# Performance work log

Measured on AMD Instinct MI355X. Metric: run time of the kernel, lower is better.

## Reference

```python
import jax, jax.numpy as jnp
import numpy as np

B, HP, WP = 4, 32, 32
T = HP * WP
C = 768            # n_embd
NH = 24            # n_head
HS = C // NH       # head_size == HEAD_SIZE == 32
E = HS             # TIME_MIX_EXTRA_DIM = HEAD_SIZE
D = 64             # TIME_DECAY_DIM


def setup_inputs() -> dict:
    key = jax.random.key(0)
    ks = jax.random.split(key, 24)
    small = lambda k, sh: jax.random.uniform(k, sh, jnp.float32, -1e-4, 1e-4)
    inp = {
        "x": jax.random.normal(ks[0], (B, T, C), jnp.float32),
        "time_maa_x": jax.random.uniform(ks[1], (1, 1, C), jnp.float32),
        "time_maa_w": jax.random.uniform(ks[2], (1, 1, C), jnp.float32),
        "time_maa_k": jax.random.uniform(ks[3], (1, 1, C), jnp.float32),
        "time_maa_v": jax.random.uniform(ks[4], (1, 1, C), jnp.float32),
        "time_maa_r": jax.random.uniform(ks[5], (1, 1, C), jnp.float32),
        "time_maa_g": jax.random.uniform(ks[6], (1, 1, C), jnp.float32),
        "time_maa_w1": small(ks[7], (C, 5 * E)),
        "time_maa_w2": small(ks[8], (5, E, C)),
        "time_decay": jnp.linspace(-6.0, -1.0, C, dtype=jnp.float32).reshape(1, 1, C),
        "time_decay_w1": small(ks[9], (C, D)),
        "time_decay_w2": small(ks[10], (D, C)),
        "time_faaaa": jax.random.uniform(ks[11], (NH, HS), jnp.float32, -0.1, 0.6),
        "W_r": jax.random.normal(ks[12], (C, C), jnp.float32) * 0.02,
        "W_k": jax.random.normal(ks[13], (C, C), jnp.float32) * 0.02,
        "W_v": jax.random.normal(ks[14], (C, C), jnp.float32) * 0.02,
        "W_g": jax.random.normal(ks[15], (C, C), jnp.float32) * 0.02,
        "W_o": jax.random.normal(ks[16], (C, C), jnp.float32) * 0.02,
        "ln_w": jnp.ones((C,), jnp.float32),
        "ln_b": jnp.zeros((C,), jnp.float32),
        "Hp": HP,
        "Wp": WP,
    }
    return inp


def q_shift(x, H, W):
    """groups_q_shift with K=1, gamma=1/4: quarter-channel 4-direction spatial shift, zero-padded."""
    Bs, Ts, Cs = x.shape
    g = x.reshape(Bs, H, W, Cs)
    c4 = Cs // 4
    a, b, c, d = g[..., :c4], g[..., c4:2 * c4], g[..., 2 * c4:3 * c4], g[..., 3 * c4:]
    a = jnp.pad(a[:, :, :-1], ((0, 0), (0, 0), (1, 0), (0, 0)))  # shift +W (right)
    b = jnp.pad(b[:, :, 1:], ((0, 0), (0, 0), (0, 1), (0, 0)))   # shift -W (left)
    c = jnp.pad(c[:, :-1], ((0, 0), (1, 0), (0, 0), (0, 0)))     # shift +H (down)
    d = jnp.pad(d[:, 1:], ((0, 0), (0, 1), (0, 0), (0, 0)))      # shift -H (up)
    return jnp.concatenate([a, b, c, d], axis=-1).reshape(Bs, Ts, Cs)


def wkv6(r, k, v, w, u):
    """RWKV6 WKV scan. r,k,v,w: (B,T,C); u: (NH,HS). decay = exp(-exp(w))."""
    Bs, Ts, Cs = r.shape
    rh = r.reshape(Bs, Ts, NH, HS)
    kh = k.reshape(Bs, Ts, NH, HS)
    vh = v.reshape(Bs, Ts, NH, HS)
    dh = jnp.exp(-jnp.exp(w)).reshape(Bs, Ts, NH, HS)

    def step(s, ins):
        rt, kt, vt, dt = ins                                   # each (B,NH,HS)
        kv = kt[..., :, None] * vt[..., None, :]               # (B,NH,HS,HS)
        y = jnp.einsum('bhj,bhji->bhi', rt, s + u[None, :, :, None] * kv)
        s = dt[..., :, None] * s + kv
        return s, y

    xs = (rh.transpose(1, 0, 2, 3), kh.transpose(1, 0, 2, 3),
          vh.transpose(1, 0, 2, 3), dh.transpose(1, 0, 2, 3))
    s0 = jnp.zeros((Bs, NH, HS, HS), r.dtype)
    _, ys = jax.lax.scan(step, s0, xs)                          # (T,B,NH,HS)
    return ys.transpose(1, 0, 2, 3).reshape(Bs, Ts, Cs)


def reference(x, time_maa_x, time_maa_w, time_maa_k, time_maa_v, time_maa_r,
              time_maa_g, time_maa_w1, time_maa_w2, time_decay, time_decay_w1,
              time_decay_w2, time_faaaa, W_r, W_k, W_v, W_g, W_o, ln_w, ln_b,
              Hp, Wp):
    Bs, Ts, Cs = x.shape
    xx = q_shift(x, Hp, Wp) - x                                 # token shift delta
    xxx = x + xx * time_maa_x
    xxx = jnp.tanh(xxx @ time_maa_w1).reshape(Bs, Ts, 5, E)
    mix = jnp.einsum('btke,kec->kbtc', xxx, time_maa_w2)        # (5,B,T,C)
    mw, mk, mv, mr, mg = mix[0], mix[1], mix[2], mix[3], mix[4]

    xw = x + xx * (time_maa_w + mw)
    xk = x + xx * (time_maa_k + mk)
    xv = x + xx * (time_maa_v + mv)
    xr = x + xx * (time_maa_r + mr)
    xg = x + xx * (time_maa_g + mg)

    r = xr @ W_r
    k = xk @ W_k
    v = xv @ W_v
    g = jax.nn.silu(xg @ W_g)

    ww = jnp.tanh(xw @ time_decay_w1) @ time_decay_w2
    w = time_decay + ww                                         # data-dependent log-decay

    y = wkv6(r, k, v, w, time_faaaa)

    # ln_x (LayerNorm over channels)
    mu = y.mean(-1, keepdims=True)
    var = ((y - mu) ** 2).mean(-1, keepdims=True)
    yn = (y - mu) / jnp.sqrt(var + 1e-5) * ln_w + ln_b

    return (yn * g) @ W_o
```

## Files before the change

### kernel.cpp

```cpp
#include <hip/hip_runtime.h>
#include <math.h>

#define BB   4
#define TT   1024
#define CC   768
#define NH_  24
#define HS_  32
#define NBH  (BB * NH_)
#define NCH  16
#define CL   64

static constexpr size_t SZ = (size_t)BB * TT * CC;

typedef __attribute__((ext_vector_type(8))) __bf16 bf16x8;
typedef __attribute__((ext_vector_type(4))) float  f32x4;

__device__ __forceinline__ unsigned short f2bf(float f) {
    unsigned u = __float_as_uint(f);
    unsigned r = (u + 0x7FFFu + ((u >> 16) & 1u)) >> 16;
    return (unsigned short)r;
}
__device__ __forceinline__ float bf2f(unsigned short h) {
    return __uint_as_float(((unsigned)h) << 16);
}

__device__ __forceinline__ void gload16(const unsigned short* g, unsigned short* l)
{
    __builtin_amdgcn_global_load_lds(
        (const __attribute__((address_space(1))) void*)(g),
        (__attribute__((address_space(3))) void*)(l),
        16, 0, 0);
}

__device__ __forceinline__ int xcd_swz(int wg, int nwg)
{
    return (wg & 7) * (nwg >> 3) + (wg >> 3);
}

struct TDesc { const float* src; unsigned short* dst; int R, C; };
struct TArgs { TDesc d[8]; };

__global__ __launch_bounds__(256) void transpose_cast(TArgs a)
{
    __shared__ float tile[32][33];
    TDesc t = a.d[blockIdx.z];
    const int tx0 = blockIdx.x * 32, ty0 = blockIdx.y * 32;
    if (tx0 >= t.C || ty0 >= t.R) return;
    const int tx = threadIdx.x & 31, ty = threadIdx.x >> 5;
    #pragma unroll
    for (int dy = 0; dy < 4; ++dy) {
        int rr = ty0 + ty + dy * 8, cc = tx0 + tx;
        tile[ty + dy * 8][tx] = (rr < t.R && cc < t.C) ? t.src[(size_t)rr * t.C + cc] : 0.f;
    }
    __syncthreads();
    #pragma unroll
    for (int dy = 0; dy < 4; ++dy) {
        int cc = tx0 + ty + dy * 8, rr = ty0 + tx;
        if (cc < t.C && rr < t.R)
            t.dst[(size_t)cc * t.R + rr] = f2bf(tile[tx][ty + dy * 8]);
    }
}

__global__ __launch_bounds__(192) void w2fill(const float* __restrict__ w2,
                                              unsigned short* __restrict__ W2t)
{
    const int n = blockIdx.x;
    const int e = threadIdx.x;
    if (e >= 160) return;
    const int kk = n / 768;
    const int c  = n - kk * 768;
    unsigned short val = 0;
    if ((e >> 5) == kk) val = f2bf(w2[(size_t)e * 768 + c]);
    W2t[(size_t)n * 160 + e] = val;
}

__global__ __launch_bounds__(256) void shift_kernel(
    const float* __restrict__ x, const float* __restrict__ maa_x,
    float* __restrict__ xxO, unsigned short* __restrict__ xxxO)
{
    const int tok = blockIdx.x;
    const int t   = tok & (TT - 1);
    const int hh  = t >> 5;
    const int wp  = t & 31;
    const int tid = threadIdx.x;
    const float* xrow = x + (size_t)tok * CC;
    for (int c = tid; c < CC; c += 256) {
        float xc = xrow[c];
        float sh;
        if (c < 192)      sh = (wp > 0)  ? xrow[c - CC]      : 0.f;
        else if (c < 384) sh = (wp < 31) ? xrow[c + CC]      : 0.f;
        else if (c < 576) sh = (hh > 0)  ? xrow[c - 32 * CC] : 0.f;
        else              sh = (hh < 31) ? xrow[c + 32 * CC] : 0.f;
        float xxv = sh - xc;
        size_t o = (size_t)tok * CC + c;
        xxO[o]  = xxv;
        xxxO[o] = f2bf(fmaf(xxv, maa_x[c], xc));
    }
}

template<int KDIM, class Epi>
__device__ __forceinline__ void gemm_core(const unsigned short* __restrict__ A,
                                          const unsigned short* __restrict__ W,
                                          int N, const Epi& epi)
{
    __shared__ __align__(16) unsigned short As[64][40];
    __shared__ __align__(16) unsigned short Bs[64][40];

    const int tid  = threadIdx.x;
    const int lane = tid & 63;
    const int wv   = tid >> 6;
    const int wm   = (wv >> 1) * 32, wn = (wv & 1) * 32;
    const int m0   = blockIdx.y * 64, n0 = blockIdx.x * 64;
    const int srow = tid >> 2, scb = (tid & 3) * 8;
    const int l15  = lane & 15, kb8 = (lane >> 4) * 8;

    f32x4 acc[2][2];
    #pragma unroll
    for (int a = 0; a < 2; ++a)
        #pragma unroll
        for (int b = 0; b < 2; ++b)
            #pragma unroll
            for (int e = 0; e < 4; ++e) acc[a][b][e] = 0.f;

    const unsigned short* aP = A + (size_t)(m0 + srow) * KDIM + scb;
    const unsigned short* bP = W + (size_t)(n0 + srow) * KDIM + scb;
    const bool bvalid = (n0 + srow) < N;

    for (int k0 = 0; k0 < KDIM; k0 += 32) {
        uint4 av = *(const uint4*)(aP + k0);
        uint4 bw = make_uint4(0u, 0u, 0u, 0u);
        if (bvalid) bw = *(const uint4*)(bP + k0);
        *(uint4*)&As[srow][scb] = av;
        *(uint4*)&Bs[srow][scb] = bw;
        __syncthreads();

        bf16x8 a0 = *(const bf16x8*)&As[wm + l15][kb8];
        bf16x8 a1 = *(const bf16x8*)&As[wm + 16 + l15][kb8];
        bf16x8 b0 = *(const bf16x8*)&Bs[wn + l15][kb8];
        bf16x8 b1 = *(const bf16x8*)&Bs[wn + 16 + l15][kb8];
        acc[0][0] = __builtin_amdgcn_mfma_f32_16x16x32_bf16(a0, b0, acc[0][0], 0, 0, 0);
        acc[0][1] = __builtin_amdgcn_mfma_f32_16x16x32_bf16(a0, b1, acc[0][1], 0, 0, 0);
        acc[1][0] = __builtin_amdgcn_mfma_f32_16x16x32_bf16(a1, b0, acc[1][0], 0, 0, 0);
        acc[1][1] = __builtin_amdgcn_mfma_f32_16x16x32_bf16(a1, b1, acc[1][1], 0, 0, 0);
        __syncthreads();
    }

    const int rb_ = m0 + wm + (lane >> 4) * 4;
    #pragma unroll
    for (int mi = 0; mi < 2; ++mi)
        #pragma unroll
        for (int ni = 0; ni < 2; ++ni) {
            int col = n0 + wn + ni * 16 + l15;
            if (col < N) {
                #pragma unroll
                for (int j = 0; j < 4; ++j)
                    epi(rb_ + mi * 16 + j, col, acc[mi][ni][j]);
            }
        }
}

template<int KDIM, int BK, class Epi>
__device__ __forceinline__ void gemm_core128(const unsigned short* __restrict__ A,
                                             const unsigned short* __restrict__ W,
                                             int N, int m0, int n0, const Epi& epi)
{
    __shared__ __align__(16) unsigned short As[128][BK];
    __shared__ __align__(16) unsigned short Bs[128][BK];

    const int tid  = threadIdx.x;
    const int lane = tid & 63;
    const int wv   = tid >> 6;
    const int wm   = (wv >> 1) * 64, wn = (wv & 1) * 64;
    const int l15  = lane & 15, kb8 = (lane >> 4) * 8, rb4 = (lane >> 4) * 4;
    constexpr int RPC = 2048 / BK;
    const int sr = tid / (BK / 8), sq = (tid % (BK / 8)) * 8;

    f32x4 acc[4][4];
    #pragma unroll
    for (int a = 0; a < 4; ++a)
        #pragma unroll
        for (int b = 0; b < 4; ++b)
            #pragma unroll
            for (int e = 0; e < 4; ++e) acc[a][b][e] = 0.f;

    const unsigned short* aP = A + (size_t)(m0 + sr) * KDIM + sq;
    const unsigned short* bP = W + (size_t)(n0 + sr) * KDIM + sq;

    for (int k0 = 0; k0 < KDIM; k0 += BK) {
        #pragma unroll
        for (int ro = 0; ro < 128; ro += RPC) {
            gload16(aP + (size_t)ro * KDIM + k0, &As[ro + sr][sq]);
            gload16(bP + (size_t)ro * KDIM + k0, &Bs[ro + sr][sq]);
        }
        __syncthreads();

        #pragma unroll
        for (int kk = 0; kk < BK; kk += 32) {
            bf16x8 af[4], bfr[4];
            #pragma unroll
            for (int mi = 0; mi < 4; ++mi)
                af[mi] = *(const bf16x8*)&As[wm + mi * 16 + l15][kk + kb8];
            #pragma unroll
            for (int ni = 0; ni < 4; ++ni)
                bfr[ni] = *(const bf16x8*)&Bs[wn + ni * 16 + l15][kk + kb8];
            #pragma unroll
            for (int mi = 0; mi < 4; ++mi)
                #pragma unroll
                for (int ni = 0; ni < 4; ++ni)
                    acc[mi][ni] = __builtin_amdgcn_mfma_f32_16x16x32_bf16(af[mi], bfr[ni], acc[mi][ni], 0, 0, 0);
        }
        __syncthreads();
    }

    const int rbase = m0 + wm + rb4;
    #pragma unroll
    for (int mi = 0; mi < 4; ++mi)
        #pragma unroll
        for (int ni = 0; ni < 4; ++ni) {
            int col = n0 + wn + ni * 16 + l15;
            if (col < N) {
                #pragma unroll
                for (int j = 0; j < 4; ++j)
                    epi(rbase + mi * 16 + j, col, acc[mi][ni][j]);
            }
        }
}

struct EpiTanh {
    unsigned short* O; int ldo;
    __device__ void operator()(int r, int c, float v) const {
        O[(size_t)r * ldo + c] = f2bf(tanhf(v));
    }
};
struct EpiF32 {
    float* O;
    __device__ void operator()(int r, int c, float v) const {
        O[(size_t)r * 768 + c] = v;
    }
};
struct EpiDec {
    const float* td; float* O;
    __device__ void operator()(int r, int c, float v) const {
        O[(size_t)r * 768 + c] = expf(-expf(td[c] + v));
    }
};
struct EpiMix {
    const float* px; const float* pxx;
    const float* maa[5];
    unsigned short* outs[5];
    __device__ void operator()(int r, int c, float v) const {
        int kk = c / 768;
        int cc = c - kk * 768;
        size_t o = (size_t)r * 768 + cc;
        outs[kk][o] = f2bf(fmaf(pxx[o], maa[kk][cc] + v, px[o]));
    }
};
struct EpiRKVG {
    unsigned short* O; bool silu;
    __device__ void operator()(int r, int c, float v) const {
        if (silu) v = v / (1.f + expf(-v));
        O[(size_t)r * 768 + c] = f2bf(v);
    }
};

template<int KDIM, class Epi>
__global__ __launch_bounds__(256) void gemm_one(const unsigned short* __restrict__ A,
                                                const unsigned short* __restrict__ W,
                                                int N, Epi epi)
{
    gemm_core<KDIM>(A, W, N, epi);
}

template<int KDIM, int BK, int NB, class Epi>
__global__ __launch_bounds__(256) void gemm_one128(const unsigned short* __restrict__ A,
                                                   const unsigned short* __restrict__ W,
                                                   int N, Epi epi)
{
    const int idx = xcd_swz(blockIdx.x, gridDim.x);
    const int m0 = (idx / NB) * 128, n0 = (idx % NB) * 128;
    gemm_core128<KDIM, BK>(A, W, N, m0, n0, epi);
}

struct QuadArgs {
    const unsigned short* A[4];
    const unsigned short* W[4];
    unsigned short* O[4];
};
__global__ __launch_bounds__(256) void gemm_quad768(QuadArgs q)
{
    const int idx = xcd_swz(blockIdx.x, 768);
    const int z = idx / 192;
    const int rz = idx - z * 192;
    const int m0 = (rz / 6) * 128, n0 = (rz % 6) * 128;
    EpiRKVG e{q.O[z], z == 3};
    gemm_core128<768, 64>(q.A[z], q.W[z], 768, m0, n0, e);
}

__global__ __launch_bounds__(256) void wkv_local(
    const unsigned short* __restrict__ r, const unsigned short* __restrict__ k,
    const unsigned short* __restrict__ v, const float* __restrict__ dec,
    const float* __restrict__ u, float* __restrict__ y,
    unsigned short* __restrict__ rsb, float* __restrict__ kvt,
    float* __restrict__ dcv)
{
    __shared__ __align__(16) unsigned short rwL[64][40], kwL[64][40];
    __shared__ __align__(16) unsigned short vT0[32][40], vT1[32][40];
    __shared__ __align__(16) unsigned short ksT0[32][40], ksT1[32][40];
    __shared__ __align__(16) unsigned short PL0[64][40], PL1[64][40];
    __shared__ float AL[65][32];
    __shared__ float segprod[8][32];
    __shared__ float dpart[64][4];
    __shared__ float diagL[64];
    __shared__ float uL[32];

    const int c   = blockIdx.x;
    const int bh  = blockIdx.y;
    const int b = bh / NH_, h = bh % NH_;
    const int tid  = threadIdx.x;
    const int lane = tid & 63;
    const int wv   = tid >> 6;
    const int l15  = lane & 15;
    const int kb8  = (lane >> 4) * 8;
    const int rb4  = (lane >> 4) * 4;
    const int tc   = c * CL;

    const size_t base0 = ((size_t)b * TT) * CC + (size_t)h * HS_;

    if (tid < 32) uL[tid] = u[h * HS_ + tid];

    const int lrow = tid >> 2, lq = (tid & 3) * 8;
    const int cj = tid & 31, cseg = tid >> 5;

    {
        size_t gp = base0 + (size_t)(tc + lrow) * CC + lq;
        uint4 rv = *(const uint4*)(r + gp);
        uint4 kv = *(const uint4*)(k + gp);
        uint4 vv = *(const uint4*)(v + gp);
        *(uint4*)&rwL[lrow][lq] = rv;
        *(uint4*)&kwL[lrow][lq] = kv;
        const unsigned short* vp = (const unsigned short*)&vv;
        if (lrow < 32) {
            #pragma unroll
            for (int e = 0; e < 8; ++e) vT0[lq + e][lrow] = vp[e];
        } else {
            #pragma unroll
            for (int e = 0; e < 8; ++e) vT1[lq + e][lrow - 32] = vp[e];
        }
    }
    float dv[8];
    #pragma unroll
    for (int q = 0; q < 8; ++q)
        dv[q] = dec[base0 + (size_t)(tc + cseg * 8 + q) * CC + cj];
    {
        float lp = dv[0];
        #pragma unroll
        for (int q = 1; q < 8; ++q) lp *= dv[q];
        segprod[cseg][cj] = lp;
    }
    __syncthreads();

    {
        const int ptau = tid >> 2, pp = tid & 3;
        float acc = 0.f;
        #pragma unroll
        for (int e = 0; e < 8; ++e) {
            int j = pp * 8 + e;
            acc += bf2f(rwL[ptau][j]) * uL[j] * bf2f(kwL[ptau][j]);
        }
        dpart[ptau][pp] = acc;
    }
    {
        float pre = 1.f;
        #pragma unroll
        for (int s = 0; s < 7; ++s) if (s < cseg) pre *= segprod[s][cj];
        float run = pre;
        #pragma unroll
        for (int q = 0; q < 8; ++q) {
            AL[cseg * 8 + q][cj] = run;
            run *= dv[q];
        }
        if (cseg == 7) AL[64][cj] = run;
    }
    __syncthreads();

    if (tid < 64)
        diagL[tid] = dpart[tid][0] + dpart[tid][1] + dpart[tid][2] + dpart[tid][3];
    if (tid < 32)
        dcv[((size_t)bh * NCH + c) * 32 + tid] = AL[64][tid];

    #pragma unroll
    for (int q = 0; q < 8; ++q) {
        int tau = cseg * 8 + q;
        float a  = AL[tau][cj];
        float ia = 1.f / AL[tau + 1][cj];
        unsigned short rs = f2bf(bf2f(rwL[tau][cj]) * a);
        unsigned short ks = f2bf(bf2f(kwL[tau][cj]) * ia);
        rwL[tau][cj] = rs;
        kwL[tau][cj] = ks;
        if (tau < 32) ksT0[cj][tau] = ks; else ksT1[cj][tau - 32] = ks;
    }
    __syncthreads();

    {
        const int wm = (wv >> 1) * 32, wn = (wv & 1) * 32;
        bf16x8 a0 = *(const bf16x8*)&rwL[wm + l15][kb8];
        bf16x8 a1 = *(const bf16x8*)&rwL[wm + 16 + l15][kb8];
        bf16x8 b0 = *(const bf16x8*)&kwL[wn + l15][kb8];
        bf16x8 b1 = *(const bf16x8*)&kwL[wn + 16 + l15][kb8];
        f32x4 qf[2][2];
        #pragma unroll
        for (int mi = 0; mi < 2; ++mi)
            #pragma unroll
            for (int ni = 0; ni < 2; ++ni)
                #pragma unroll
                for (int e = 0; e < 4; ++e) qf[mi][ni][e] = 0.f;
        qf[0][0] = __builtin_amdgcn_mfma_f32_16x16x32_bf16(a0, b0, qf[0][0], 0, 0, 0);
        qf[0][1] = __builtin_amdgcn_mfma_f32_16x16x32_bf16(a0, b1, qf[0][1], 0, 0, 0);
        qf[1][0] = __builtin_amdgcn_mfma_f32_16x16x32_bf16(a1, b0, qf[1][0], 0, 0, 0);
        qf[1][1] = __builtin_amdgcn_mfma_f32_16x16x32_bf16(a1, b1, qf[1][1], 0, 0, 0);
        #pragma unroll
        for (int mi = 0; mi < 2; ++mi)
            #pragma unroll
            for (int ni = 0; ni < 2; ++ni) {
                const int col = wn + ni * 16 + l15;
                #pragma unroll
                for (int jj = 0; jj < 4; ++jj) {
                    const int row = wm + mi * 16 + rb4 + jj;
                    float val = (col < row) ? qf[mi][ni][jj]
                              : ((col == row) ? diagL[row] : 0.f);
                    unsigned short bvv = f2bf(val);
                    if (col < 32) PL0[row][col] = bvv;
                    else          PL1[row][col - 32] = bvv;
                }
            }
    }
    __syncthreads();

    *(uint4*)(rsb + base0 + (size_t)(tc + lrow) * CC + lq) = *(const uint4*)&rwL[lrow][lq];

    {
        const int mr = wv * 16;
        bf16x8 pa0 = *(const bf16x8*)&PL0[mr + l15][kb8];
        bf16x8 pa1 = *(const bf16x8*)&PL1[mr + l15][kb8];
        #pragma unroll
        for (int ni = 0; ni < 2; ++ni) {
            bf16x8 bv0 = *(const bf16x8*)&vT0[ni * 16 + l15][kb8];
            bf16x8 bv1 = *(const bf16x8*)&vT1[ni * 16 + l15][kb8];
            f32x4 acc;
            #pragma unroll
            for (int e = 0; e < 4; ++e) acc[e] = 0.f;
            acc = __builtin_amdgcn_mfma_f32_16x16x32_bf16(pa0, bv0, acc, 0, 0, 0);
            acc = __builtin_amdgcn_mfma_f32_16x16x32_bf16(pa1, bv1, acc, 0, 0, 0);
            #pragma unroll
            for (int jj = 0; jj < 4; ++jj)
                y[base0 + (size_t)(tc + mr + rb4 + jj) * CC + ni * 16 + l15] = acc[jj];
        }
    }

    {
        const int mi_ = (wv >> 1) * 16, nj = (wv & 1) * 16;
        bf16x8 av0 = *(const bf16x8*)&vT0[mi_ + l15][kb8];
        bf16x8 av1 = *(const bf16x8*)&vT1[mi_ + l15][kb8];
        bf16x8 bk0 = *(const bf16x8*)&ksT0[nj + l15][kb8];
        bf16x8 bk1 = *(const bf16x8*)&ksT1[nj + l15][kb8];
        f32x4 acc;
        #pragma unroll
        for (int e = 0; e < 4; ++e) acc[e] = 0.f;
        acc = __builtin_amdgcn_mfma_f32_16x16x32_bf16(av0, bk0, acc, 0, 0, 0);
        acc = __builtin_amdgcn_mfma_f32_16x16x32_bf16(av1, bk1, acc, 0, 0, 0);
        const int j = nj + l15;
        const size_t sb = ((size_t)bh * NCH + c) << 10;
        #pragma unroll
        for (int jj = 0; jj < 4; ++jj)
            kvt[sb + (size_t)(mi_ + rb4 + jj) * 32 + j] = acc[jj];
    }
}

__global__ __launch_bounds__(256) void wkv_carry(
    const float* __restrict__ kvt, const float* __restrict__ dcv,
    unsigned short* __restrict__ spv)
{
    const int bh = blockIdx.x;
    const int tid = threadIdx.x;
    const int e0 = tid << 2;
    const int j0 = e0 & 31;
    float s0 = 0.f, s1 = 0.f, s2 = 0.f, s3 = 0.f;
    #pragma unroll
    for (int c = 0; c < NCH; ++c) {
        const size_t sb = (size_t)bh * NCH + c;
        float4 kv = *(const float4*)(kvt + (sb << 10) + e0);
        float4 d4 = *(const float4*)(dcv + sb * 32 + j0);
        s0 = d4.x * (s0 + kv.x);
        s1 = d4.y * (s1 + kv.y);
        s2 = d4.z * (s2 + kv.z);
        s3 = d4.w * (s3 + kv.w);
        if (c < NCH - 1) {
            unsigned lo = (unsigned)f2bf(s0) | ((unsigned)f2bf(s1) << 16);
            unsigned hi = (unsigned)f2bf(s2) | ((unsigned)f2bf(s3) << 16);
            *(uint2*)(spv + ((sb + 1) << 10) + e0) = make_uint2(lo, hi);
        }
    }
}

__global__ __launch_bounds__(256) void wkv_stadd(
    const unsigned short* __restrict__ rsb, const unsigned short* __restrict__ spv,
    float* __restrict__ y)
{
    __shared__ __align__(16) unsigned short rsL[64][40];
    __shared__ __align__(16) unsigned short STb[32][40];

    const int c  = blockIdx.x + 1;
    const int bh = blockIdx.y;
    const int b = bh / NH_, h = bh % NH_;
    const int tid = threadIdx.x, lane = tid & 63, wv = tid >> 6;
    const int l15 = lane & 15, kb8 = (lane >> 4) * 8, rb4 = (lane >> 4) * 4;
    const int tc = c * CL;
    const size_t base0 = ((size_t)b * TT) * CC + (size_t)h * HS_;
    const int lrow = tid >> 2, lq = (tid & 3) * 8;

    *(uint4*)&rsL[lrow][lq] = *(const uint4*)(rsb + base0 + (size_t)(tc + lrow) * CC + lq);
    if (tid < 128) {
        int row = tid >> 2, q = (tid & 3) * 8;
        *(uint4*)&STb[row][q] =
            *(const uint4*)(spv + (((size_t)bh * NCH + c) << 10) + (size_t)row * 32 + q);
    }
    __syncthreads();

    const int mr = wv * 16;
    bf16x8 ra = *(const bf16x8*)&rsL[mr + l15][kb8];
    #pragma unroll
    for (int ni = 0; ni < 2; ++ni) {
        bf16x8 bs = *(const bf16x8*)&STb[ni * 16 + l15][kb8];
        f32x4 acc;
        #pragma unroll
        for (int e = 0; e < 4; ++e) acc[e] = 0.f;
        acc = __builtin_amdgcn_mfma_f32_16x16x32_bf16(ra, bs, acc, 0, 0, 0);
        #pragma unroll
        for (int jj = 0; jj < 4; ++jj) {
            size_t gp = base0 + (size_t)(tc + mr + rb4 + jj) * CC + ni * 16 + l15;
            y[gp] += acc[jj];
        }
    }
}

__global__ __launch_bounds__(256) void ln_gate(
    const float* __restrict__ y, const unsigned short* __restrict__ g,
    const float* __restrict__ lnw, const float* __restrict__ lnb,
    unsigned short* __restrict__ z)
{
    __shared__ float sy[CC];
    __shared__ float rbuf[8];
    __shared__ float stats[2];

    const int row = blockIdx.x, tid = threadIdx.x;
    const float* yr = y + (size_t)row * CC;

    float s1 = 0.f, s2 = 0.f;
    #pragma unroll
    for (int q = 0; q < 3; ++q) {
        int c = tid + q * 256;
        float vv = yr[c];
        sy[c] = vv;
        s1 += vv;
        s2 += vv * vv;
    }
    #pragma unroll
    for (int off = 32; off > 0; off >>= 1) {
        s1 += __shfl_down(s1, off);
        s2 += __shfl_down(s2, off);
    }
    const int wid = tid >> 6;
    if ((tid & 63) == 0) { rbuf[wid] = s1; rbuf[4 + wid] = s2; }
    __syncthreads();
    if (tid == 0) {
        float S1 = rbuf[0] + rbuf[1] + rbuf[2] + rbuf[3];
        float S2 = rbuf[4] + rbuf[5] + rbuf[6] + rbuf[7];
        float mu = S1 / (float)CC;
        float var = S2 / (float)CC - mu * mu;
        stats[0] = mu;
        stats[1] = rsqrtf(var + 1e-5f);
    }
    __syncthreads();
    const float mu = stats[0], rstd = stats[1];
    const unsigned short* gr = g + (size_t)row * CC;
    unsigned short* zr = z + (size_t)row * CC;
    #pragma unroll
    for (int q = 0; q < 3; ++q) {
        int c = tid + q * 256;
        zr[c] = f2bf(fmaf((sy[c] - mu) * rstd, lnw[c], lnb[c]) * bf2f(gr[c]));
    }
}

extern "C" void kernel_launch(void* const* d_in, const int* in_sizes, int n_in,
                              void* d_out, int out_size, void* d_ws, size_t ws_size,
                              hipStream_t stream)
{
    const float* x      = (const float*)d_in[0];
    const float* maa_x  = (const float*)d_in[1];
    const float* maa_w  = (const float*)d_in[2];
    const float* maa_k  = (const float*)d_in[3];
    const float* maa_v  = (const float*)d_in[4];
    const float* maa_r  = (const float*)d_in[5];
    const float* maa_g  = (const float*)d_in[6];
    const float* w1     = (const float*)d_in[7];
    const float* w2     = (const float*)d_in[8];
    const float* tdec   = (const float*)d_in[9];
    const float* tdw1   = (const float*)d_in[10];
    const float* tdw2   = (const float*)d_in[11];
    const float* faaaa  = (const float*)d_in[12];
    const float* Wr     = (const float*)d_in[13];
    const float* Wk     = (const float*)d_in[14];
    const float* Wv     = (const float*)d_in[15];
    const float* Wg     = (const float*)d_in[16];
    const float* Wo     = (const float*)d_in[17];
    const float* lnw    = (const float*)d_in[18];
    const float* lnb    = (const float*)d_in[19];

    char* base = (char*)d_ws;
    size_t off = 0;
    auto alloc = [&](size_t bytes) -> char* {
        char* p = base + off;
        off = (off + bytes + 255) & ~(size_t)255;
        return p;
    };

    float*          xx   = (float*)alloc(SZ * 4);
    float*          decb = (float*)alloc(SZ * 4);
    unsigned short* xxx  = (unsigned short*)alloc(SZ * 2);
    unsigned short* xw   = (unsigned short*)alloc(SZ * 2);
    unsigned short* xk   = (unsigned short*)alloc(SZ * 2);
    unsigned short* xv   = (unsigned short*)alloc(SZ * 2);
    unsigned short* xr   = (unsigned short*)alloc(SZ * 2);
    unsigned short* xg   = (unsigned short*)alloc(SZ * 2);
    unsigned short* rb   = (unsigned short*)alloc(SZ * 2);
    unsigned short* kb   = (unsigned short*)alloc(SZ * 2);
    unsigned short* vb   = (unsigned short*)alloc(SZ * 2);
    unsigned short* gb   = (unsigned short*)alloc(SZ * 2);
    unsigned short* t5   = (unsigned short*)alloc((size_t)4096 * 160 * 2);
    unsigned short* d1   = (unsigned short*)alloc((size_t)4096 * 64 * 2);
    unsigned short* w1t  = (unsigned short*)alloc((size_t)160 * 768 * 2);
    unsigned short* w2t  = (unsigned short*)alloc((size_t)3840 * 160 * 2);
    unsigned short* wrt  = (unsigned short*)alloc((size_t)768 * 768 * 2);
    unsigned short* wkt  = (unsigned short*)alloc((size_t)768 * 768 * 2);
    unsigned short* wvt  = (unsigned short*)alloc((size_t)768 * 768 * 2);
    unsigned short* wgt  = (unsigned short*)alloc((size_t)768 * 768 * 2);
    unsigned short* wot  = (unsigned short*)alloc((size_t)768 * 768 * 2);
    unsigned short* td1t = (unsigned short*)alloc((size_t)64 * 768 * 2);
    unsigned short* td2t = (unsigned short*)alloc((size_t)768 * 64 * 2);

    float*          y    = xx;
    unsigned short* z    = xxx;
    unsigned short* rsb  = xr;
    float*          kvtb = (float*)xk;
    unsigned short* spvb = xv;
    float*          dcb  = (float*)xg;

    TArgs ta = {{
        { w1,   w1t,  768, 160 },
        { Wr,   wrt,  768, 768 },
        { Wk,   wkt,  768, 768 },
        { Wv,   wvt,  768, 768 },
        { Wg,   wgt,  768, 768 },
        { Wo,   wot,  768, 768 },
        { tdw1, td1t, 768, 64  },
        { tdw2, td2t, 64,  768 },
    }};
    transpose_cast<<<dim3(24, 24, 8), 256, 0, stream>>>(ta);
    w2fill<<<3840, 192, 0, stream>>>(w2, w2t);

    shift_kernel<<<BB * TT, 256, 0, stream>>>(x, maa_x, xx, xxx);

    gemm_one<768, EpiTanh><<<dim3(3, 64), 256, 0, stream>>>(xxx, w1t, 160, EpiTanh{t5, 160});

    EpiMix em{ x, xx,
               { maa_w, maa_k, maa_v, maa_r, maa_g },
               { xw, xk, xv, xr, xg } };
    gemm_one128<160, 32, 30, EpiMix><<<960, 256, 0, stream>>>(t5, w2t, 3840, em);

    gemm_one<768, EpiTanh><<<dim3(1, 64), 256, 0, stream>>>(xw, td1t, 64, EpiTanh{d1, 64});

    gemm_one<64, EpiDec><<<dim3(12, 64), 256, 0, stream>>>(d1, td2t, 768, EpiDec{tdec, decb});

    QuadArgs qa = {{ xr, xk, xv, xg }, { wrt, wkt, wvt, wgt }, { rb, kb, vb, gb }};
    gemm_quad768<<<768, 256, 0, stream>>>(qa);

    wkv_local<<<dim3(NCH, NBH), 256, 0, stream>>>(rb, kb, vb, decb, faaaa, y, rsb, kvtb, dcb);
    wkv_carry<<<NBH, 256, 0, stream>>>(kvtb, dcb, spvb);
    wkv_stadd<<<dim3(NCH - 1, NBH), 256, 0, stream>>>(rsb, spvb, y);

    ln_gate<<<BB * TT, 256, 0, stream>>>(y, gb, lnw, lnb, z);

    gemm_one128<768, 64, 6, EpiF32><<<192, 256, 0, stream>>>(z, wot, 768, EpiF32{(float*)d_out});
}
```

Measured before the change: 270.4 us.

## Fuse state-add into LayerNorm, merge w2fill, async LDS loads, smaller K-tiles

Folds the w2 fill kernel into the transpose_cast launch as an extra z-slice. The small GEMM core now uses global_load_lds direct-to-LDS loads with unpadded tiles and clamps out-of-range B rows instead of zero-filling them. The quad and output GEMMs switch to a BK of 32. The wkv_stadd kernel is removed and its inter-chunk state contribution is computed inside the LayerNorm kernel as a per-channel dot product, which saves a launch and a read-modify-write of y but adds scalar FMA work and repeated state reads per row. Unpadded LDS tiles may add bank conflicts, and clamped B rows load real data into tiles that were previously zero.

```diff
diff --git a/kernel.cpp b/kernel.cpp
--- a/kernel.cpp
+++ b/kernel.cpp
@@ -38,15 +38,30 @@
 }
 
 struct TDesc { const float* src; unsigned short* dst; int R, C; };
-struct TArgs { TDesc d[8]; };
+struct TArgs { TDesc d[8]; const float* w2; unsigned short* W2t; };
 
 __global__ __launch_bounds__(256) void transpose_cast(TArgs a)
 {
+    const int tid = threadIdx.x;
+    if (blockIdx.z == 8) {
+        const int wid = blockIdx.y * 24 + blockIdx.x;
+        if (wid >= 480) return;
+        for (int idx = tid; idx < 8 * 160; idx += 256) {
+            const int n = wid * 8 + (idx / 160);
+            const int e = idx - (idx / 160) * 160;
+            const int kk = n / 768;
+            const int cc = n - kk * 768;
+            unsigned short val = 0;
+            if ((e >> 5) == kk) val = f2bf(a.w2[(size_t)e * 768 + cc]);
+            a.W2t[(size_t)n * 160 + e] = val;
+        }
+        return;
+    }
     __shared__ float tile[32][33];
     TDesc t = a.d[blockIdx.z];
     const int tx0 = blockIdx.x * 32, ty0 = blockIdx.y * 32;
     if (tx0 >= t.C || ty0 >= t.R) return;
-    const int tx = threadIdx.x & 31, ty = threadIdx.x >> 5;
+    const int tx = tid & 31, ty = tid >> 5;
     #pragma unroll
     for (int dy = 0; dy < 4; ++dy) {
         int rr = ty0 + ty + dy * 8, cc = tx0 + tx;
@@ -59,19 +74,6 @@
         if (cc < t.C && rr < t.R)
             t.dst[(size_t)cc * t.R + rr] = f2bf(tile[tx][ty + dy * 8]);
     }
-}
-
-__global__ __launch_bounds__(192) void w2fill(const float* __restrict__ w2,
-                                              unsigned short* __restrict__ W2t)
-{
-    const int n = blockIdx.x;
-    const int e = threadIdx.x;
-    if (e >= 160) return;
-    const int kk = n / 768;
-    const int c  = n - kk * 768;
-    unsigned short val = 0;
-    if ((e >> 5) == kk) val = f2bf(w2[(size_t)e * 768 + c]);
-    W2t[(size_t)n * 160 + e] = val;
 }
 
 __global__ __launch_bounds__(256) void shift_kernel(
@@ -103,8 +105,8 @@
                                           const unsigned short* __restrict__ W,
                                           int N, const Epi& epi)
 {
-    __shared__ __align__(16) unsigned short As[64][40];
-    __shared__ __align__(16) unsigned short Bs[64][40];
+    __shared__ __align__(16) unsigned short As[64][32];
+    __shared__ __align__(16) unsigned short Bs[64][32];
 
     const int tid  = threadIdx.x;
     const int lane = tid & 63;
@@ -122,16 +124,13 @@
             #pragma unroll
             for (int e = 0; e < 4; ++e) acc[a][b][e] = 0.f;
 
+    int brow = n0 + srow; if (brow > N - 1) brow = N - 1;
     const unsigned short* aP = A + (size_t)(m0 + srow) * KDIM + scb;
-    const unsigned short* bP = W + (size_t)(n0 + srow) * KDIM + scb;
-    const bool bvalid = (n0 + srow) < N;
+    const unsigned short* bP = W + (size_t)brow * KDIM + scb;
 
     for (int k0 = 0; k0 < KDIM; k0 += 32) {
-        uint4 av = *(const uint4*)(aP + k0);
-        uint4 bw = make_uint4(0u, 0u, 0u, 0u);
-        if (bvalid) bw = *(const uint4*)(bP + k0);
-        *(uint4*)&As[srow][scb] = av;
-        *(uint4*)&Bs[srow][scb] = bw;
+        gload16(aP + k0, &As[srow][scb]);
+        gload16(bP + k0, &Bs[srow][scb]);
         __syncthreads();
 
         bf16x8 a0 = *(const bf16x8*)&As[wm + l15][kb8];
@@ -293,7 +292,7 @@
     const int rz = idx - z * 192;
     const int m0 = (rz / 6) * 128, n0 = (rz % 6) * 128;
     EpiRKVG e{q.O[z], z == 3};
-    gemm_core128<768, 64>(q.A[z], q.W[z], 768, m0, n0, e);
+    gemm_core128<768, 32>(q.A[z], q.W[z], 768, m0, n0, e);
 }
 
 __global__ __launch_bounds__(256) void wkv_local(
@@ -502,64 +501,47 @@
     }
 }
 
-__global__ __launch_bounds__(256) void wkv_stadd(
-    const unsigned short* __restrict__ rsb, const unsigned short* __restrict__ spv,
-    float* __restrict__ y)
-{
-    __shared__ __align__(16) unsigned short rsL[64][40];
-    __shared__ __align__(16) unsigned short STb[32][40];
-
-    const int c  = blockIdx.x + 1;
-    const int bh = blockIdx.y;
-    const int b = bh / NH_, h = bh % NH_;
-    const int tid = threadIdx.x, lane = tid & 63, wv = tid >> 6;
-    const int l15 = lane & 15, kb8 = (lane >> 4) * 8, rb4 = (lane >> 4) * 4;
-    const int tc = c * CL;
-    const size_t base0 = ((size_t)b * TT) * CC + (size_t)h * HS_;
-    const int lrow = tid >> 2, lq = (tid & 3) * 8;
-
-    *(uint4*)&rsL[lrow][lq] = *(const uint4*)(rsb + base0 + (size_t)(tc + lrow) * CC + lq);
-    if (tid < 128) {
-        int row = tid >> 2, q = (tid & 3) * 8;
-        *(uint4*)&STb[row][q] =
-            *(const uint4*)(spv + (((size_t)bh * NCH + c) << 10) + (size_t)row * 32 + q);
-    }
-    __syncthreads();
-
-    const int mr = wv * 16;
-    bf16x8 ra = *(const bf16x8*)&rsL[mr + l15][kb8];
-    #pragma unroll
-    for (int ni = 0; ni < 2; ++ni) {
-        bf16x8 bs = *(const bf16x8*)&STb[ni * 16 + l15][kb8];
-        f32x4 acc;
-        #pragma unroll
-        for (int e = 0; e < 4; ++e) acc[e] = 0.f;
-        acc = __builtin_amdgcn_mfma_f32_16x16x32_bf16(ra, bs, acc, 0, 0, 0);
-        #pragma unroll
-        for (int jj = 0; jj < 4; ++jj) {
-            size_t gp = base0 + (size_t)(tc + mr + rb4 + jj) * CC + ni * 16 + l15;
-            y[gp] += acc[jj];
-        }
-    }
-}
-
-__global__ __launch_bounds__(256) void ln_gate(
-    const float* __restrict__ y, const unsigned short* __restrict__ g,
+__global__ __launch_bounds__(256) void ln_gate_fused(
+    const float* __restrict__ y, const unsigned short* __restrict__ rsb,
+    const unsigned short* __restrict__ spv, const unsigned short* __restrict__ g,
     const float* __restrict__ lnw, const float* __restrict__ lnb,
     unsigned short* __restrict__ z)
 {
     __shared__ float sy[CC];
+    __shared__ unsigned short rs[CC];
     __shared__ float rbuf[8];
     __shared__ float stats[2];
 
     const int row = blockIdx.x, tid = threadIdx.x;
+    const int b = row >> 10;
+    const int t = row & 1023;
+    const int chunk = t >> 6;
     const float* yr = y + (size_t)row * CC;
+
+    if (tid < 96)
+        *(uint4*)&rs[tid * 8] = *(const uint4*)(rsb + (size_t)row * CC + tid * 8);
+    __syncthreads();
 
     float s1 = 0.f, s2 = 0.f;
     #pragma unroll
     for (int q = 0; q < 3; ++q) {
         int c = tid + q * 256;
         float vv = yr[c];
+        if (chunk > 0) {
+            const int h = c >> 5, i = c & 31;
+            const unsigned short* sp =
+                spv + ((((size_t)(b * NH_ + h)) * NCH + chunk) << 10) + (size_t)i * 32;
+            float add = 0.f;
+            #pragma unroll
+            for (int qq = 0; qq < 4; ++qq) {
+                uint4 sv = *(const uint4*)(sp + qq * 8);
+                const unsigned short* s8 = (const unsigned short*)&sv;
+                #pragma unroll
+                for (int j = 0; j < 8; ++j)
+                    add = fmaf(bf2f(rs[h * 32 + qq * 8 + j]), bf2f(s8[j]), add);
+            }
+            vv += add;
+        }
         sy[c] = vv;
         s1 += vv;
         s2 += vv * vv;
@@ -664,9 +646,8 @@
         { Wo,   wot,  768, 768 },
         { tdw1, td1t, 768, 64  },
         { tdw2, td2t, 64,  768 },
-    }};
-    transpose_cast<<<dim3(24, 24, 8), 256, 0, stream>>>(ta);
-    w2fill<<<3840, 192, 0, stream>>>(w2, w2t);
+    }, w2, w2t};
+    transpose_cast<<<dim3(24, 24, 9), 256, 0, stream>>>(ta);
 
     shift_kernel<<<BB * TT, 256, 0, stream>>>(x, maa_x, xx, xxx);
 
@@ -686,9 +667,8 @@
 
     wkv_local<<<dim3(NCH, NBH), 256, 0, stream>>>(rb, kb, vb, decb, faaaa, y, rsb, kvtb, dcb);
     wkv_carry<<<NBH, 256, 0, stream>>>(kvtb, dcb, spvb);
-    wkv_stadd<<<dim3(NCH - 1, NBH), 256, 0, stream>>>(rsb, spvb, y);
-
-    ln_gate<<<BB * TT, 256, 0, stream>>>(y, gb, lnw, lnb, z);
-
-    gemm_one128<768, 64, 6, EpiF32><<<192, 256, 0, stream>>>(z, wot, 768, EpiF32{(float*)d_out});
-}
+
+    ln_gate_fused<<<BB * TT, 256, 0, stream>>>(y, rsb, spvb, gb, lnw, lnb, z);
+
+    gemm_one128<768, 32, 6, EpiF32><<<192, 256, 0, stream>>>(z, wot, 768, EpiF32{(float*)d_out});
+}
```

New measurement: 279.9 us. 1.04x slower.
